# Kernel optimization log

Measured on AMD Instinct MI355X. Metric: run time of the kernel, lower is better.

The kernel has to match this reference:

```python
import jax, jax.numpy as jnp
import numpy as np

# Model dims (match init_kwargs)
D_MODEL = 768
D_STATE = 128
HEADDIM = 64
EXPAND = 2
D_CONV = 4
D_INNER = EXPAND * D_MODEL              # 1536 (== d_ssm)
NHEADS = D_INNER // HEADDIM             # 24
CONV_DIM = D_INNER + 2 * D_STATE        # 1792
D_IN_PROJ = 2 * D_INNER + 2 * D_STATE + NHEADS  # 3352
BATCH, SEQLEN = 2, 512


def setup_inputs() -> dict:
    key = jax.random.key(0)
    ks = jax.random.split(key, 8)
    u = jax.random.normal(ks[0], (BATCH, SEQLEN, D_MODEL), jnp.float32)
    W_in = jax.random.normal(ks[1], (D_IN_PROJ, D_MODEL), jnp.float32) * 0.02
    conv_w = jax.random.normal(ks[2], (CONV_DIM, D_CONV), jnp.float32) * 0.3
    conv_b = jax.random.normal(ks[3], (CONV_DIM,), jnp.float32) * 0.1
    # dt_bias = inverse-softplus of dt sampled log-uniform in [dt_min, dt_max]
    dt = jnp.exp(jax.random.uniform(ks[4], (NHEADS,)) * (np.log(0.02) - np.log(1e-3)) + np.log(1e-3))
    dt_bias = dt + jnp.log(-jnp.expm1(-dt))
    A_log = jnp.log(jax.random.uniform(ks[5], (NHEADS,), minval=1.0, maxval=16.0))
    D_param = jnp.ones((NHEADS,), jnp.float32)
    W_out = jax.random.normal(ks[6], (D_MODEL, D_INNER), jnp.float32) * 0.02
    return dict(u=u, W_in=W_in, conv_w=conv_w, conv_b=conv_b,
                dt_bias=dt_bias, A_log=A_log, D_param=D_param, W_out=W_out)


def _mamba2_scan(u, W_in, conv_w, conv_b, dt_bias, A_log, D_param, W_out):
    B, L, _ = u.shape
    A = -jnp.exp(A_log)  # (H,)

    def step(carry, u_t):
        conv_state, ssm_state = carry  # (B, CONV_DIM, D_CONV), (B, H, P, N)
        zxbcdt = u_t @ W_in.T          # (B, D_IN_PROJ); d_mlp == 0
        z = zxbcdt[:, :D_INNER]
        xBC = zxbcdt[:, D_INNER:D_INNER + CONV_DIM]
        dt = zxbcdt[:, D_INNER + CONV_DIM:]
        # causal depthwise conv state update (roll + write last)
        conv_state = jnp.concatenate([conv_state[:, :, 1:], xBC[:, :, None]], axis=-1)
        xbc = jax.nn.silu(jnp.sum(conv_state * conv_w[None], axis=-1) + conv_b)
        x = xbc[:, :D_INNER]
        Bm = xbc[:, D_INNER:D_INNER + D_STATE]
        Cm = xbc[:, D_INNER + D_STATE:]
        dt = jax.nn.softplus(dt + dt_bias)          # (B, H)
        dA = jnp.exp(dt * A)                        # (B, H)
        xh = x.reshape(B, NHEADS, HEADDIM)          # (B, H, P)
        dBx = jnp.einsum('bh,bn,bhp->bhpn', dt, Bm, xh)
        ssm_state = ssm_state * dA[:, :, None, None] + dBx
        y = jnp.einsum('bhpn,bn->bhp', ssm_state, Cm) + D_param[None, :, None] * xh
        y = y.reshape(B, D_INNER) * jax.nn.silu(z)  # gate (rmsnorm=False)
        return (conv_state, ssm_state), y @ W_out.T

    init = (jnp.zeros((B, CONV_DIM, D_CONV), u.dtype),
            jnp.zeros((B, NHEADS, HEADDIM, D_STATE), u.dtype))
    _, ys = jax.lax.scan(jax.checkpoint(step), init, jnp.swapaxes(u, 0, 1))
    return jnp.swapaxes(ys, 0, 1)  # (B, L, D_MODEL)


def reference(u, W_in, conv_w, conv_b, dt_bias, A_log, D_param, W_out):
    return _mamba2_scan(u, W_in, conv_w, conv_b, dt_bias, A_log, D_param, W_out)
```

## Files before the change

### kernel.cpp

```cpp
#include <hip/hip_runtime.h>
#include <math.h>

#define B_     2
#define L_     512
#define DM     768
#define DS     128
#define HD     64
#define DI     1536
#define NH     24
#define CONVD  1792
#define DPROJ  3352
#define ML     (B_*L_)
#define Q      64
#define NC     (L_/Q)
#define NPAD1  3456

typedef __bf16 bf16x8 __attribute__((ext_vector_type(8)));
typedef float f32x4 __attribute__((ext_vector_type(4)));

__device__ __forceinline__ float sigmoidf_(float x){ return 1.f/(1.f+__expf(-x)); }
__device__ __forceinline__ ushort bf16rn(float x){
  uint u = __float_as_uint(x);
  u += 0x7fff + ((u>>16)&1);
  return (ushort)(u>>16);
}
__device__ __forceinline__ float bf2f(ushort h){ return __uint_as_float(((uint)h)<<16); }
__device__ __forceinline__ void gll16(const void* g, void* l){
  __builtin_amdgcn_global_load_lds((const __attribute__((address_space(1))) void*)g,
                                   (__attribute__((address_space(3))) void*)l, 16, 0, 0);
}

__launch_bounds__(256)
__global__ void cvt_split(const float* __restrict__ src, ushort* __restrict__ dst,
                          int Rsrc, int Rdst, int K){
  int idx = blockIdx.x*256 + threadIdx.x;
  int K4 = K>>2;
  if (idx >= Rdst*K4) return;
  int r = idx / K4, c = (idx - r*K4)<<2;
  float4 v = make_float4(0,0,0,0);
  if (r < Rsrc) v = *(const float4*)&src[(size_t)r*K + c];
  float xv[4] = {v.x,v.y,v.z,v.w};
  uint hp[2], lp[2];
  ushort h[4], l[4];
#pragma unroll
  for (int j=0;j<4;j++){ h[j]=bf16rn(xv[j]); l[j]=bf16rn(xv[j]-bf2f(h[j])); }
  hp[0] = (uint)h[0] | ((uint)h[1]<<16); hp[1] = (uint)h[2] | ((uint)h[3]<<16);
  lp[0] = (uint)l[0] | ((uint)l[1]<<16); lp[1] = (uint)l[2] | ((uint)l[3]<<16);
  *(uint2*)&dst[(size_t)r*2*K + c]     = make_uint2(hp[0],hp[1]);
  *(uint2*)&dst[(size_t)r*2*K + K + c] = make_uint2(lp[0],lp[1]);
}

template<int BM,int BN,int K,int SPLITK,bool ATOMIC>
__launch_bounds__(256, 2)
__global__ void gemm4(const ushort* __restrict__ AS, const ushort* __restrict__ BS,
                      float* __restrict__ C, int Nvalid, int Nstore){
  constexpr int KS = K / SPLITK;
  constexpr int STEPS = KS / 64;
  constexpr int WM=BM/2, WN=BN/2, FM=WM/16, FN=WN/16;
  __shared__ ushort Ah[2][BM*64], Alo[2][BM*64], Bh[2][BN*64], Blo[2][BN*64];
  const int tid=threadIdx.x, lane=tid&63, w=tid>>6;
  const int WR=w>>1, WC=w&1;
  const int bm=blockIdx.x*BM, bn=blockIdx.y*BN;
  const int kbase = blockIdx.z*KS;
  const int lr=lane&15;
  const int srow=lane>>3;
  const int scol=(((lane&7) ^ (srow&7))*8);
  f32x4 acc[FM][FN] = {};

  auto stage = [&](int d, int ks){
    int k0 = kbase + ks*64;
#pragma unroll
    for (int ci=w; ci<BM/8; ci+=4){
      size_t ro = (size_t)(bm + ci*8 + srow)*(2*K);
      gll16(&AS[ro + k0 + scol],     &Ah[d][ci*512]);
      gll16(&AS[ro + K + k0 + scol], &Alo[d][ci*512]);
    }
#pragma unroll
    for (int ci=w; ci<BN/8; ci+=4){
      size_t ro = (size_t)(bn + ci*8 + srow)*(2*K);
      gll16(&BS[ro + k0 + scol],     &Bh[d][ci*512]);
      gll16(&BS[ro + K + k0 + scol], &Blo[d][ci*512]);
    }
  };

  stage(0, 0);
  __syncthreads();
  int cur = 0;
  for (int ks=0; ks<STEPS; ks++){
    if (ks+1 < STEPS) stage(cur^1, ks+1);

    bf16x8 ah[2][FM], al[2][FM], bh[2][FN], bl[2][FN];
#pragma unroll
    for (int s2=0;s2<2;s2++){
      int gslot = s2*4 + (lane>>4);
#pragma unroll
      for (int i=0;i<FM;i++){
        int R = WR*WM + i*16 + lr;
        int so = (gslot ^ (lr&7))*8;
        ah[s2][i] = *(const bf16x8*)&Ah[cur][R*64 + so];
        al[s2][i] = *(const bf16x8*)&Alo[cur][R*64 + so];
      }
#pragma unroll
      for (int j=0;j<FN;j++){
        int R = WC*WN + j*16 + lr;
        int so = (gslot ^ (lr&7))*8;
        bh[s2][j] = *(const bf16x8*)&Bh[cur][R*64 + so];
        bl[s2][j] = *(const bf16x8*)&Blo[cur][R*64 + so];
      }
    }
#pragma unroll
    for (int s2=0;s2<2;s2++)
#pragma unroll
      for (int i=0;i<FM;i++)
#pragma unroll
        for (int j=0;j<FN;j++){
          acc[i][j] = __builtin_amdgcn_mfma_f32_16x16x32_bf16(ah[s2][i], bh[s2][j], acc[i][j], 0,0,0);
          acc[i][j] = __builtin_amdgcn_mfma_f32_16x16x32_bf16(ah[s2][i], bl[s2][j], acc[i][j], 0,0,0);
          acc[i][j] = __builtin_amdgcn_mfma_f32_16x16x32_bf16(al[s2][i], bh[s2][j], acc[i][j], 0,0,0);
        }

    __syncthreads();
    cur ^= 1;
  }

#pragma unroll
  for (int i=0;i<FM;i++)
#pragma unroll
    for (int j=0;j<FN;j++){
      int n = bn + WC*WN + j*16 + lr;
      if (n < Nvalid){
#pragma unroll
        for (int e=0;e<4;e++){
          int m = bm + WR*WM + i*16 + (lane>>4)*4 + e;
          if (ATOMIC) atomicAdd(&C[(size_t)m*Nstore + n], acc[i][j][e]);
          else        C[(size_t)m*Nstore + n] = acc[i][j][e];
        }
      }
    }
}

__launch_bounds__(256)
__global__ void conv2_kernel(const float* __restrict__ zx,
                             const float* __restrict__ cw,
                             const float* __restrict__ cb,
                             float* __restrict__ xbc){
  int g = blockIdx.x;
  int c2 = blockIdx.y;
  int b = blockIdx.z;
  int t0g = c2*32;
  int ch = g*256 + threadIdx.x;
  const float* src = zx + (size_t)(b*L_ + t0g)*DPROJ + DI + ch;
  float* dst = xbc + (size_t)(b*L_ + t0g)*CONVD + ch;
  float w0=cw[ch*4],w1=cw[ch*4+1],w2=cw[ch*4+2],w3=cw[ch*4+3],bias=cb[ch];
  float x0=0.f,x1=0.f,x2=0.f;
  if (t0g > 0){
    x0 = *(src - 3*DPROJ);
    x1 = *(src - 2*DPROJ);
    x2 = *(src - 1*DPROJ);
  }
#pragma unroll 4
  for (int tt=0; tt<32; tt++){
    float xt = src[(size_t)tt*DPROJ];
    float a = bias;
    a = fmaf(w3, xt, a); a = fmaf(w2, x2, a); a = fmaf(w1, x1, a); a = fmaf(w0, x0, a);
    dst[(size_t)tt*CONVD] = a * sigmoidf_(a);
    x0 = x1; x1 = x2; x2 = xt;
  }
}

__launch_bounds__(64)
__global__ void dt_kernel(const float* __restrict__ zx,
                          const float* __restrict__ dt_bias,
                          const float* __restrict__ A_log,
                          float* __restrict__ dts, float* __restrict__ las){
  int blk = blockIdx.x;
  int c = blk % NC; int h = (blk/NC)%NH; int b = blk/(NC*NH);
  int lane = threadIdx.x;
  int t = c*Q + lane;
  float raw = zx[(size_t)(b*L_+t)*DPROJ + DI + CONVD + h] + dt_bias[h];
  float dtv = raw > 20.f ? raw : log1pf(__expf(raw));
  float A = -__expf(A_log[h]);
  float la = dtv * A;
#pragma unroll
  for (int off=1; off<64; off<<=1){
    float v = __shfl_up(la, off);
    if (lane >= off) la += v;
  }
  int idx = (b*NH+h)*L_ + t;
  dts[idx] = dtv;
  las[idx] = la;
}

__launch_bounds__(256)
__global__ void chunk_state_kernel(const float* __restrict__ xbc,
                                   const float* __restrict__ dts,
                                   const float* __restrict__ las,
                                   float* __restrict__ Schunk){
  __shared__ float Xw[Q][68];
  __shared__ float Bs[Q][132];
  int c = blockIdx.x, h = blockIdx.y, b = blockIdx.z;
  int tid = threadIdx.x;
  int bh = b*NH + h;
  const int tbase = bh*L_ + c*Q;
  float la63 = las[tbase + 63];

  for (int it = tid; it < Q*16; it += 256){
    int s = it >> 4, p4 = (it & 15) << 2;
    float4 v = *(const float4*)&xbc[(size_t)(b*L_ + c*Q + s)*CONVD + h*HD + p4];
    float w = __expf(la63 - las[tbase + s]) * dts[tbase + s];
    Xw[s][p4+0]=v.x*w; Xw[s][p4+1]=v.y*w; Xw[s][p4+2]=v.z*w; Xw[s][p4+3]=v.w*w;
  }
  for (int it = tid; it < Q*32; it += 256){
    int s = it >> 5, n4 = (it & 31) << 2;
    float4 v = *(const float4*)&xbc[(size_t)(b*L_ + c*Q + s)*CONVD + DI + n4];
    Bs[s][n4+0]=v.x; Bs[s][n4+1]=v.y; Bs[s][n4+2]=v.z; Bs[s][n4+3]=v.w;
  }
  __syncthreads();

  int ty = tid >> 4, tx = tid & 15;
  int p0 = ty*4;
  float acc[4][8] = {};
#pragma unroll 4
  for (int k=0;k<Q;k++){
    float4 a4 = *(const float4*)&Xw[k][p0];
    float4 b0 = *(const float4*)&Bs[k][tx*4];
    float4 b1 = *(const float4*)&Bs[k][64 + tx*4];
    float a[4]={a4.x,a4.y,a4.z,a4.w};
    float bb[8]={b0.x,b0.y,b0.z,b0.w,b1.x,b1.y,b1.z,b1.w};
#pragma unroll
    for(int i=0;i<4;i++)
#pragma unroll
      for(int j=0;j<8;j++) acc[i][j] = fmaf(a[i], bb[j], acc[i][j]);
  }
  float* Sb = Schunk + ((size_t)bh*NC + c)*(HD*DS);
#pragma unroll
  for(int i=0;i<4;i++){
    int p = p0+i;
    *(float4*)&Sb[p*DS + tx*4]      = make_float4(acc[i][0],acc[i][1],acc[i][2],acc[i][3]);
    *(float4*)&Sb[p*DS + 64 + tx*4] = make_float4(acc[i][4],acc[i][5],acc[i][6],acc[i][7]);
  }
}

__launch_bounds__(256)
__global__ void interchunk_kernel(float* __restrict__ S, const float* __restrict__ las){
  int blk = blockIdx.x;
  int slice = blk & 7; int bh = blk >> 3;
  size_t base = (size_t)bh*NC*(HD*DS) + slice*1024 + threadIdx.x*4;
  float4 run = make_float4(0,0,0,0);
#pragma unroll
  for (int c=0;c<NC;c++){
    float dec = __expf(las[bh*L_ + c*Q + 63]);
    float4 ch = *(float4*)(S + base + c*(HD*DS));
    *(float4*)(S + base + c*(HD*DS)) = run;
    run.x = fmaf(run.x, dec, ch.x);
    run.y = fmaf(run.y, dec, ch.y);
    run.z = fmaf(run.z, dec, ch.z);
    run.w = fmaf(run.w, dec, ch.w);
  }
}

__launch_bounds__(512)
__global__ void chunk_out_mfma(const float* __restrict__ zx,
                               const float* __restrict__ xbc,
                               const float* __restrict__ dts,
                               const float* __restrict__ las,
                               const float* __restrict__ Sstart,
                               const float* __restrict__ Dp,
                               ushort* __restrict__ yS){
  constexpr int OC_HI = 0,      OC_LO = 8192;
  constexpr int OP_HI = 16384,  OP_LO = 24576;
  constexpr int OX_HI = 32768,  OX_LO = 36864;
  constexpr int OG_HI = 40960,  OG_LO = 45056;
  __shared__ ushort LDSU[49152];
  __shared__ float La[64], Dt[64];

  int c = blockIdx.x, hh = blockIdx.y, b = blockIdx.z;
  int tid = threadIdx.x;
  int bh = b*NH + hh;
  const int tbase = bh*L_ + c*Q;
  const float Dh = Dp[hh];
  const int lane = tid & 63, w = tid >> 6;
  const int wr = w >> 2, wc = w & 3;
  const int lr = lane & 15, lk = lane >> 4;

  for (int it = tid; it < 64*32; it += 512){
    int t = it >> 5, n4 = (it & 31) << 2;
    float4 v = *(const float4*)&xbc[(size_t)(b*L_ + c*Q + t)*CONVD + DI + DS + n4];
    float xv[4] = {v.x,v.y,v.z,v.w};
    ushort h[4], l[4];
#pragma unroll
    for (int j=0;j<4;j++){ h[j]=bf16rn(xv[j]); l[j]=bf16rn(xv[j]-bf2f(h[j])); }
    int idx = t*128 + (((n4>>3) ^ (t&7))<<3) + (n4&7);
    *(uint2*)&LDSU[OC_HI + idx] = make_uint2((uint)h[0]|((uint)h[1]<<16), (uint)h[2]|((uint)h[3]<<16));
    *(uint2*)&LDSU[OC_LO + idx] = make_uint2((uint)l[0]|((uint)l[1]<<16), (uint)l[2]|((uint)l[3]<<16));
  }
  const float* Sb = Sstart + ((size_t)bh*NC + c)*(HD*DS);
  for (int it = tid; it < 64*32; it += 512){
    int p = it >> 5, n4 = (it & 31) << 2;
    float4 v = *(const float4*)&Sb[p*DS + n4];
    float xv[4] = {v.x,v.y,v.z,v.w};
    ushort h[4], l[4];
#pragma unroll
    for (int j=0;j<4;j++){ h[j]=bf16rn(xv[j]); l[j]=bf16rn(xv[j]-bf2f(h[j])); }
    int idx = p*128 + (((n4>>3) ^ (p&7))<<3) + (n4&7);
    *(uint2*)&LDSU[OP_HI + idx] = make_uint2((uint)h[0]|((uint)h[1]<<16), (uint)h[2]|((uint)h[3]<<16));
    *(uint2*)&LDSU[OP_LO + idx] = make_uint2((uint)l[0]|((uint)l[1]<<16), (uint)l[2]|((uint)l[3]<<16));
  }
  for (int it = tid; it < 64*16; it += 512){
    int s = it >> 4, p4 = (it & 15) << 2;
    float4 v = *(const float4*)&xbc[(size_t)(b*L_ + c*Q + s)*CONVD + hh*HD + p4];
    float xv[4] = {v.x,v.y,v.z,v.w};
#pragma unroll
    for (int j=0;j<4;j++){
      int p = p4 + j;
      ushort h = bf16rn(xv[j]);
      ushort l = bf16rn(xv[j] - bf2f(h));
      int idx = p*64 + (((s>>3) ^ (p&7))<<3) + (s&7);
      LDSU[OX_HI + idx] = h; LDSU[OX_LO + idx] = l;
    }
  }
  if (tid < 64){ La[tid] = las[tbase + tid]; Dt[tid] = dts[tbase + tid]; }
  __syncthreads();

  f32x4 yi[2] = {}, ev[2] = {}, yv[2] = {};

#pragma unroll
  for (int ks=0; ks<4; ks++){
    bf16x8 ah[2], al[2], bh, bl;
#pragma unroll
    for (int fi=0; fi<2; fi++){
      int R = wr*32 + fi*16 + lr;
      int idx = R*128 + (((ks*4 + lk) ^ (R&7))<<3);
      ah[fi] = *(const bf16x8*)&LDSU[OC_HI + idx];
      al[fi] = *(const bf16x8*)&LDSU[OC_LO + idx];
    }
    { int Rb = wc*16 + lr;
      int idx = Rb*128 + (((ks*4 + lk) ^ (Rb&7))<<3);
      bh = *(const bf16x8*)&LDSU[OP_HI + idx];
      bl = *(const bf16x8*)&LDSU[OP_LO + idx]; }
#pragma unroll
    for (int fi=0; fi<2; fi++){
      yi[fi] = __builtin_amdgcn_mfma_f32_16x16x32_bf16(ah[fi], bh, yi[fi], 0,0,0);
      yi[fi] = __builtin_amdgcn_mfma_f32_16x16x32_bf16(ah[fi], bl, yi[fi], 0,0,0);
      yi[fi] = __builtin_amdgcn_mfma_f32_16x16x32_bf16(al[fi], bh, yi[fi], 0,0,0);
    }
  }
  __syncthreads();

  for (int it = tid; it < 64*32; it += 512){
    int s = it >> 5, n4 = (it & 31) << 2;
    float4 v = *(const float4*)&xbc[(size_t)(b*L_ + c*Q + s)*CONVD + DI + n4];
    float xv[4] = {v.x,v.y,v.z,v.w};
    ushort h[4], l[4];
#pragma unroll
    for (int j=0;j<4;j++){ h[j]=bf16rn(xv[j]); l[j]=bf16rn(xv[j]-bf2f(h[j])); }
    int idx = s*128 + (((n4>>3) ^ (s&7))<<3) + (n4&7);
    *(uint2*)&LDSU[OP_HI + idx] = make_uint2((uint)h[0]|((uint)h[1]<<16), (uint)h[2]|((uint)h[3]<<16));
    *(uint2*)&LDSU[OP_LO + idx] = make_uint2((uint)l[0]|((uint)l[1]<<16), (uint)l[2]|((uint)l[3]<<16));
  }
  __syncthreads();

#pragma unroll
  for (int ks=0; ks<4; ks++){
    bf16x8 ah[2], al[2], bh, bl;
#pragma unroll
    for (int fi=0; fi<2; fi++){
      int R = wr*32 + fi*16 + lr;
      int idx = R*128 + (((ks*4 + lk) ^ (R&7))<<3);
      ah[fi] = *(const bf16x8*)&LDSU[OC_HI + idx];
      al[fi] = *(const bf16x8*)&LDSU[OC_LO + idx];
    }
    { int Rb = wc*16 + lr;
      int idx = Rb*128 + (((ks*4 + lk) ^ (Rb&7))<<3);
      bh = *(const bf16x8*)&LDSU[OP_HI + idx];
      bl = *(const bf16x8*)&LDSU[OP_LO + idx]; }
#pragma unroll
    for (int fi=0; fi<2; fi++){
      ev[fi] = __builtin_amdgcn_mfma_f32_16x16x32_bf16(ah[fi], bh, ev[fi], 0,0,0);
      ev[fi] = __builtin_amdgcn_mfma_f32_16x16x32_bf16(ah[fi], bl, ev[fi], 0,0,0);
      ev[fi] = __builtin_amdgcn_mfma_f32_16x16x32_bf16(al[fi], bh, ev[fi], 0,0,0);
    }
  }

  {
    int s_col = wc*16 + lr;
    float las_s = La[s_col], dt_s = Dt[s_col];
#pragma unroll
    for (int fi=0; fi<2; fi++)
#pragma unroll
      for (int e=0; e<4; e++){
        int t = wr*32 + fi*16 + lk*4 + e;
        float g = 0.f;
        if (s_col <= t) g = __expf(La[t] - las_s) * dt_s * ev[fi][e];
        ushort hg = bf16rn(g);
        ushort lg = bf16rn(g - bf2f(hg));
        int idx = t*64 + (((s_col>>3) ^ (t&7))<<3) + (s_col&7);
        LDSU[OG_HI + idx] = hg; LDSU[OG_LO + idx] = lg;
      }
  }
  __syncthreads();

#pragma unroll
  for (int ks=0; ks<2; ks++){
    bf16x8 ah[2], al[2], bh, bl;
#pragma unroll
    for (int fi=0; fi<2; fi++){
      int R = wr*32 + fi*16 + lr;
      int idx = R*64 + (((ks*4 + lk) ^ (R&7))<<3);
      ah[fi] = *(const bf16x8*)&LDSU[OG_HI + idx];
      al[fi] = *(const bf16x8*)&LDSU[OG_LO + idx];
    }
    { int Rb = wc*16 + lr;
      int idx = Rb*64 + (((ks*4 + lk) ^ (Rb&7))<<3);
      bh = *(const bf16x8*)&LDSU[OX_HI + idx];
      bl = *(const bf16x8*)&LDSU[OX_LO + idx]; }
#pragma unroll
    for (int fi=0; fi<2; fi++){
      yv[fi] = __builtin_amdgcn_mfma_f32_16x16x32_bf16(ah[fi], bh, yv[fi], 0,0,0);
      yv[fi] = __builtin_amdgcn_mfma_f32_16x16x32_bf16(ah[fi], bl, yv[fi], 0,0,0);
      yv[fi] = __builtin_amdgcn_mfma_f32_16x16x32_bf16(al[fi], bh, yv[fi], 0,0,0);
    }
  }
  __syncthreads();

  {
    float* Yf = (float*)&LDSU[OG_HI];
    int p = wc*16 + lr;
#pragma unroll
    for (int fi=0; fi<2; fi++)
#pragma unroll
      for (int e=0; e<4; e++){
        int t = wr*32 + fi*16 + lk*4 + e;
        Yf[t*64 + p] = __expf(La[t])*yi[fi][e] + yv[fi][e];
      }
  }
  __syncthreads();

  {
    const float* Yf = (const float*)&LDSU[OG_HI];
    for (int it = tid; it < 64*16; it += 512){
      int t = it >> 4, p4 = (it & 15) << 2;
      size_t row = (size_t)(b*L_ + c*Q + t);
      float4 x4 = *(const float4*)&xbc[row*CONVD + hh*HD + p4];
      float4 z4 = *(const float4*)&zx[row*DPROJ + hh*HD + p4];
      float xx[4] = {x4.x,x4.y,x4.z,x4.w};
      float zz[4] = {z4.x,z4.y,z4.z,z4.w};
      ushort h4[4], l4[4];
#pragma unroll
      for (int j=0;j<4;j++){
        float y = Yf[t*64 + p4 + j] + Dh*xx[j];
        float o = y * (zz[j] * sigmoidf_(zz[j]));
        h4[j] = bf16rn(o);
        l4[j] = bf16rn(o - bf2f(h4[j]));
      }
      size_t o0 = row*(size_t)(2*DI) + hh*HD + p4;
      *(uint2*)&yS[o0]      = make_uint2((uint)h4[0]|((uint)h4[1]<<16), (uint)h4[2]|((uint)h4[3]<<16));
      *(uint2*)&yS[o0 + DI] = make_uint2((uint)l4[0]|((uint)l4[1]<<16), (uint)l4[2]|((uint)l4[3]<<16));
    }
  }
}

extern "C" void kernel_launch(void* const* d_in, const int* in_sizes, int n_in,
                              void* d_out, int out_size, void* d_ws, size_t ws_size,
                              hipStream_t stream) {
  const float* u       = (const float*)d_in[0];
  const float* W_in    = (const float*)d_in[1];
  const float* conv_w  = (const float*)d_in[2];
  const float* conv_b  = (const float*)d_in[3];
  const float* dt_bias = (const float*)d_in[4];
  const float* A_log   = (const float*)d_in[5];
  const float* D_param = (const float*)d_in[6];
  const float* W_out   = (const float*)d_in[7];
  float* out = (float*)d_out;

  float* ws = (float*)d_ws;
  float* zx     = ws;
  float* xbc    = zx   + (size_t)ML*DPROJ;
  float* dts    = xbc  + (size_t)ML*CONVD;
  float* las    = dts  + (size_t)B_*NH*L_;
  float* Schunk = las  + (size_t)B_*NH*L_;
  ushort* uS    = (ushort*)(Schunk + (size_t)B_*NH*NC*HD*DS);
  ushort* yS    = uS;
  ushort* WinS  = yS + (size_t)ML*2*DI;
  ushort* WoutS = WinS;

  cvt_split<<<(ML*(DM/4)+255)/256, 256, 0, stream>>>(u, uS, ML, ML, DM);
  cvt_split<<<(NPAD1*(DM/4)+255)/256, 256, 0, stream>>>(W_in, WinS, DPROJ, NPAD1, DM);
  {
    dim3 grid(ML/64, NPAD1/64, 1);
    gemm4<64,64,DM,1,false><<<grid, 256, 0, stream>>>(uS, WinS, zx, DPROJ, DPROJ);
  }
  {
    dim3 grid(7, L_/32, B_);
    conv2_kernel<<<grid, 256, 0, stream>>>(zx, conv_w, conv_b, xbc);
  }
  dt_kernel<<<B_*NH*NC, 64, 0, stream>>>(zx, dt_bias, A_log, dts, las);
  {
    dim3 grid(NC, NH, B_);
    chunk_state_kernel<<<grid, 256, 0, stream>>>(xbc, dts, las, Schunk);
  }
  interchunk_kernel<<<B_*NH*8, 256, 0, stream>>>(Schunk, las);
  {
    dim3 grid(NC, NH, B_);
    chunk_out_mfma<<<grid, 512, 0, stream>>>(zx, xbc, dts, las, Schunk, D_param, yS);
  }
  cvt_split<<<(DM*(DI/4)+255)/256, 256, 0, stream>>>(W_out, WoutS, DM, DM, DI);
  hipMemsetAsync(d_out, 0, (size_t)out_size*sizeof(float), stream);
  {
    dim3 grid(ML/64, DM/64, 4);
    gemm4<64,64,DI,4,true><<<grid, 256, 0, stream>>>(yS, WoutS, out, DM, DM);
  }
}
```

Before: 183.4 us.

## Fuse conversions and output zeroing; fold dt into chunk_state, switch it to MFMA

```diff
diff --git a/kernel.cpp b/kernel.cpp
--- a/kernel.cpp
+++ b/kernel.cpp
@@ -30,24 +30,41 @@
                                    (__attribute__((address_space(3))) void*)l, 16, 0, 0);
 }
 
+__device__ __forceinline__ void cvt4(const float* srcp, ushort* dsth, ushort* dstl, bool valid){
+  float4 v = valid ? *(const float4*)srcp : make_float4(0,0,0,0);
+  float xv[4] = {v.x,v.y,v.z,v.w};
+  ushort h[4], l[4];
+#pragma unroll
+  for (int j=0;j<4;j++){ h[j]=bf16rn(xv[j]); l[j]=bf16rn(xv[j]-bf2f(h[j])); }
+  *(uint2*)dsth = make_uint2((uint)h[0]|((uint)h[1]<<16), (uint)h[2]|((uint)h[3]<<16));
+  *(uint2*)dstl = make_uint2((uint)l[0]|((uint)l[1]<<16), (uint)l[2]|((uint)l[3]<<16));
+}
+
 __launch_bounds__(256)
-__global__ void cvt_split(const float* __restrict__ src, ushort* __restrict__ dst,
-                          int Rsrc, int Rdst, int K){
+__global__ void cvt_all(const float* __restrict__ u, const float* __restrict__ W_in,
+                        const float* __restrict__ W_out,
+                        ushort* __restrict__ uS, ushort* __restrict__ WinS,
+                        ushort* __restrict__ WoutS, float* __restrict__ out, int outN4){
+  const int N1 = ML*(DM/4);
+  const int N2 = NPAD1*(DM/4);
+  const int N3 = DM*(DI/4);
   int idx = blockIdx.x*256 + threadIdx.x;
-  int K4 = K>>2;
-  if (idx >= Rdst*K4) return;
-  int r = idx / K4, c = (idx - r*K4)<<2;
-  float4 v = make_float4(0,0,0,0);
-  if (r < Rsrc) v = *(const float4*)&src[(size_t)r*K + c];
-  float xv[4] = {v.x,v.y,v.z,v.w};
-  uint hp[2], lp[2];
-  ushort h[4], l[4];
-#pragma unroll
-  for (int j=0;j<4;j++){ h[j]=bf16rn(xv[j]); l[j]=bf16rn(xv[j]-bf2f(h[j])); }
-  hp[0] = (uint)h[0] | ((uint)h[1]<<16); hp[1] = (uint)h[2] | ((uint)h[3]<<16);
-  lp[0] = (uint)l[0] | ((uint)l[1]<<16); lp[1] = (uint)l[2] | ((uint)l[3]<<16);
-  *(uint2*)&dst[(size_t)r*2*K + c]     = make_uint2(hp[0],hp[1]);
-  *(uint2*)&dst[(size_t)r*2*K + K + c] = make_uint2(lp[0],lp[1]);
+  if (idx < N1){
+    int r = idx/(DM/4), c = (idx - r*(DM/4))<<2;
+    cvt4(&u[(size_t)r*DM + c], &uS[(size_t)r*2*DM + c], &uS[(size_t)r*2*DM + DM + c], true);
+  } else if (idx < N1+N2){
+    int li = idx - N1;
+    int r = li/(DM/4), c = (li - r*(DM/4))<<2;
+    bool valid = r < DPROJ;
+    cvt4(&W_in[(size_t)(valid ? r : 0)*DM + c], &WinS[(size_t)r*2*DM + c], &WinS[(size_t)r*2*DM + DM + c], valid);
+  } else if (idx < N1+N2+N3){
+    int li = idx - N1 - N2;
+    int r = li/(DI/4), c = (li - r*(DI/4))<<2;
+    cvt4(&W_out[(size_t)r*DI + c], &WoutS[(size_t)r*2*DI + c], &WoutS[(size_t)r*2*DI + DI + c], true);
+  } else {
+    int o = idx - (N1+N2+N3);
+    if (o < outN4) *(float4*)&out[(size_t)o*4] = make_float4(0,0,0,0);
+  }
 }
 
 template<int BM,int BN,int K,int SPLITK,bool ATOMIC>
@@ -168,77 +185,112 @@
   }
 }
 
-__launch_bounds__(64)
-__global__ void dt_kernel(const float* __restrict__ zx,
-                          const float* __restrict__ dt_bias,
-                          const float* __restrict__ A_log,
-                          float* __restrict__ dts, float* __restrict__ las){
-  int blk = blockIdx.x;
-  int c = blk % NC; int h = (blk/NC)%NH; int b = blk/(NC*NH);
-  int lane = threadIdx.x;
-  int t = c*Q + lane;
-  float raw = zx[(size_t)(b*L_+t)*DPROJ + DI + CONVD + h] + dt_bias[h];
-  float dtv = raw > 20.f ? raw : log1pf(__expf(raw));
-  float A = -__expf(A_log[h]);
-  float la = dtv * A;
-#pragma unroll
-  for (int off=1; off<64; off<<=1){
-    float v = __shfl_up(la, off);
-    if (lane >= off) la += v;
-  }
-  int idx = (b*NH+h)*L_ + t;
-  dts[idx] = dtv;
-  las[idx] = la;
-}
-
 __launch_bounds__(256)
-__global__ void chunk_state_kernel(const float* __restrict__ xbc,
-                                   const float* __restrict__ dts,
-                                   const float* __restrict__ las,
-                                   float* __restrict__ Schunk){
-  __shared__ float Xw[Q][68];
-  __shared__ float Bs[Q][132];
-  int c = blockIdx.x, h = blockIdx.y, b = blockIdx.z;
-  int tid = threadIdx.x;
-  int bh = b*NH + h;
-  const int tbase = bh*L_ + c*Q;
-  float la63 = las[tbase + 63];
-
-  for (int it = tid; it < Q*16; it += 256){
+__global__ void chunk_state_mfma(const float* __restrict__ zx,
+                                 const float* __restrict__ xbc,
+                                 const float* __restrict__ dt_bias,
+                                 const float* __restrict__ A_log,
+                                 float* __restrict__ dts, float* __restrict__ las,
+                                 float* __restrict__ Schunk){
+  constexpr int OX_HI=0, OX_LO=4096;
+  constexpr int OB_HI=8192, OB_LO=16384;
+  __shared__ ushort L[24576];
+  __shared__ float Wt[64];
+  int c=blockIdx.x, h=blockIdx.y, b=blockIdx.z;
+  int tid=threadIdx.x;
+  int bh=b*NH+h;
+  const int tbase=bh*L_+c*Q;
+
+  if (tid < 64){
+    int t = c*Q + tid;
+    float raw = zx[(size_t)(b*L_+t)*DPROJ + DI + CONVD + h] + dt_bias[h];
+    float dtv = raw > 20.f ? raw : log1pf(__expf(raw));
+    float A = -__expf(A_log[h]);
+    float la = dtv*A;
+#pragma unroll
+    for (int off=1; off<64; off<<=1){
+      float v = __shfl_up(la, off);
+      if (tid >= off) la += v;
+    }
+    dts[tbase + tid] = dtv;
+    las[tbase + tid] = la;
+    float la63 = __shfl(la, 63);
+    Wt[tid] = __expf(la63 - la) * dtv;
+  }
+  __syncthreads();
+
+  for (int it = tid; it < 64*16; it += 256){
     int s = it >> 4, p4 = (it & 15) << 2;
     float4 v = *(const float4*)&xbc[(size_t)(b*L_ + c*Q + s)*CONVD + h*HD + p4];
-    float w = __expf(la63 - las[tbase + s]) * dts[tbase + s];
-    Xw[s][p4+0]=v.x*w; Xw[s][p4+1]=v.y*w; Xw[s][p4+2]=v.z*w; Xw[s][p4+3]=v.w*w;
-  }
-  for (int it = tid; it < Q*32; it += 256){
+    float ws = Wt[s];
+    float xv[4] = {v.x*ws, v.y*ws, v.z*ws, v.w*ws};
+#pragma unroll
+    for (int j=0;j<4;j++){
+      int p = p4 + j;
+      ushort hh = bf16rn(xv[j]);
+      ushort ll = bf16rn(xv[j] - bf2f(hh));
+      int idx = p*64 + (((s>>3) ^ (p&7))<<3) + (s&7);
+      L[OX_HI + idx] = hh; L[OX_LO + idx] = ll;
+    }
+  }
+  for (int it = tid; it < 64*32; it += 256){
     int s = it >> 5, n4 = (it & 31) << 2;
     float4 v = *(const float4*)&xbc[(size_t)(b*L_ + c*Q + s)*CONVD + DI + n4];
-    Bs[s][n4+0]=v.x; Bs[s][n4+1]=v.y; Bs[s][n4+2]=v.z; Bs[s][n4+3]=v.w;
-  }
-  __syncthreads();
-
-  int ty = tid >> 4, tx = tid & 15;
-  int p0 = ty*4;
-  float acc[4][8] = {};
-#pragma unroll 4
-  for (int k=0;k<Q;k++){
-    float4 a4 = *(const float4*)&Xw[k][p0];
-    float4 b0 = *(const float4*)&Bs[k][tx*4];
-    float4 b1 = *(const float4*)&Bs[k][64 + tx*4];
-    float a[4]={a4.x,a4.y,a4.z,a4.w};
-    float bb[8]={b0.x,b0.y,b0.z,b0.w,b1.x,b1.y,b1.z,b1.w};
-#pragma unroll
-    for(int i=0;i<4;i++)
-#pragma unroll
-      for(int j=0;j<8;j++) acc[i][j] = fmaf(a[i], bb[j], acc[i][j]);
-  }
+    float xv[4] = {v.x,v.y,v.z,v.w};
+#pragma unroll
+    for (int j=0;j<4;j++){
+      int n = n4 + j;
+      ushort hh = bf16rn(xv[j]);
+      ushort ll = bf16rn(xv[j] - bf2f(hh));
+      int idx = n*64 + (((s>>3) ^ (n&7))<<3) + (s&7);
+      L[OB_HI + idx] = hh; L[OB_LO + idx] = ll;
+    }
+  }
+  __syncthreads();
+
+  const int lane = tid & 63, w = tid >> 6;
+  const int wr = w >> 1, wc = w & 1;
+  const int lr = lane & 15, lk = lane >> 4;
+  f32x4 acc[2][4] = {};
+#pragma unroll
+  for (int ks=0; ks<2; ks++){
+    bf16x8 ah[2], al[2], bhf[4], blf[4];
+#pragma unroll
+    for (int fi=0; fi<2; fi++){
+      int R = wr*32 + fi*16 + lr;
+      int idx = R*64 + (((ks*4 + lk) ^ (R&7))<<3);
+      ah[fi] = *(const bf16x8*)&L[OX_HI + idx];
+      al[fi] = *(const bf16x8*)&L[OX_LO + idx];
+    }
+#pragma unroll
+    for (int fj=0; fj<4; fj++){
+      int Rb = wc*64 + fj*16 + lr;
+      int idx = Rb*64 + (((ks*4 + lk) ^ (Rb&7))<<3);
+      bhf[fj] = *(const bf16x8*)&L[OB_HI + idx];
+      blf[fj] = *(const bf16x8*)&L[OB_LO + idx];
+    }
+#pragma unroll
+    for (int fi=0; fi<2; fi++)
+#pragma unroll
+      for (int fj=0; fj<4; fj++){
+        acc[fi][fj] = __builtin_amdgcn_mfma_f32_16x16x32_bf16(ah[fi], bhf[fj], acc[fi][fj], 0,0,0);
+        acc[fi][fj] = __builtin_amdgcn_mfma_f32_16x16x32_bf16(ah[fi], blf[fj], acc[fi][fj], 0,0,0);
+        acc[fi][fj] = __builtin_amdgcn_mfma_f32_16x16x32_bf16(al[fi], bhf[fj], acc[fi][fj], 0,0,0);
+      }
+  }
+
   float* Sb = Schunk + ((size_t)bh*NC + c)*(HD*DS);
 #pragma unroll
-  for(int i=0;i<4;i++){
-    int p = p0+i;
-    *(float4*)&Sb[p*DS + tx*4]      = make_float4(acc[i][0],acc[i][1],acc[i][2],acc[i][3]);
-    *(float4*)&Sb[p*DS + 64 + tx*4] = make_float4(acc[i][4],acc[i][5],acc[i][6],acc[i][7]);
-  }
+  for (int fi=0; fi<2; fi++)
+#pragma unroll
+    for (int fj=0; fj<4; fj++){
+      int n = wc*64 + fj*16 + lr;
+#pragma unroll
+      for (int e=0; e<4; e++){
+        int p = wr*32 + fi*16 + lk*4 + e;
+        Sb[p*DS + n] = acc[fi][fj][e];
+      }
+    }
 }
 
 __launch_bounds__(256)
@@ -481,11 +533,14 @@
   float* Schunk = las  + (size_t)B_*NH*L_;
   ushort* uS    = (ushort*)(Schunk + (size_t)B_*NH*NC*HD*DS);
   ushort* yS    = uS;
-  ushort* WinS  = yS + (size_t)ML*2*DI;
-  ushort* WoutS = WinS;
-
-  cvt_split<<<(ML*(DM/4)+255)/256, 256, 0, stream>>>(u, uS, ML, ML, DM);
-  cvt_split<<<(NPAD1*(DM/4)+255)/256, 256, 0, stream>>>(W_in, WinS, DPROJ, NPAD1, DM);
+  ushort* WinS  = uS + (size_t)ML*2*DI;
+  ushort* WoutS = WinS + (size_t)NPAD1*2*DM;
+
+  {
+    int outN4 = out_size/4;
+    int total = ML*(DM/4) + NPAD1*(DM/4) + DM*(DI/4) + outN4;
+    cvt_all<<<(total+255)/256, 256, 0, stream>>>(u, W_in, W_out, uS, WinS, WoutS, out, outN4);
+  }
   {
     dim3 grid(ML/64, NPAD1/64, 1);
     gemm4<64,64,DM,1,false><<<grid, 256, 0, stream>>>(uS, WinS, zx, DPROJ, DPROJ);
@@ -494,18 +549,15 @@
     dim3 grid(7, L_/32, B_);
     conv2_kernel<<<grid, 256, 0, stream>>>(zx, conv_w, conv_b, xbc);
   }
-  dt_kernel<<<B_*NH*NC, 64, 0, stream>>>(zx, dt_bias, A_log, dts, las);
   {
     dim3 grid(NC, NH, B_);
-    chunk_state_kernel<<<grid, 256, 0, stream>>>(xbc, dts, las, Schunk);
+    chunk_state_mfma<<<grid, 256, 0, stream>>>(zx, xbc, dt_bias, A_log, dts, las, Schunk);
   }
   interchunk_kernel<<<B_*NH*8, 256, 0, stream>>>(Schunk, las);
   {
     dim3 grid(NC, NH, B_);
     chunk_out_mfma<<<grid, 512, 0, stream>>>(zx, xbc, dts, las, Schunk, D_param, yS);
   }
-  cvt_split<<<(DM*(DI/4)+255)/256, 256, 0, stream>>>(W_out, WoutS, DM, DM, DI);
-  hipMemsetAsync(d_out, 0, (size_t)out_size*sizeof(float), stream);
   {
     dim3 grid(ML/64, DM/64, 4);
     gemm4<64,64,DI,4,true><<<grid, 256, 0, stream>>>(yS, WoutS, out, DM, DM);
```

Result: faster. 175.3 us (-4.4%).
